# Kernel tuning notes

Hardware: AMD Instinct MI355X
Metric: run time of the kernel (lower is better)

The kernel has to match this reference:

```python
import math
import jax, jax.numpy as jnp
import numpy as np

B, S, E, H = 4, 2048, 1024, 16
HD = E // H  # 64


def setup_inputs() -> dict:
    key = jax.random.key(0)
    ks = jax.random.split(key, 7)
    scale = 1.0 / math.sqrt(E)
    return {
        "x": jax.random.normal(ks[0], (B, S, E), dtype=jnp.float32),
        "Wq": jax.random.normal(ks[1], (H, HD, E), dtype=jnp.float32) * scale,
        "bq": jax.random.normal(ks[2], (H, HD), dtype=jnp.float32) * 0.01,
        "Wk": jax.random.normal(ks[3], (H, HD, E), dtype=jnp.float32) * scale,
        "bk": jax.random.normal(ks[4], (H, HD), dtype=jnp.float32) * 0.01,
        "Wv": jax.random.normal(ks[5], (H, HD, E), dtype=jnp.float32) * scale,
        "bv": jax.random.normal(ks[6], (H, HD), dtype=jnp.float32) * 0.01,
    }


def reference(x, Wq, bq, Wk, bk, Wv, bv):
    b, s, e = x.shape
    h, hd, _ = Wq.shape
    inv_scale = 1.0 / math.sqrt(hd)
    # per-head linear projections (torch Linear: x @ W^T + b), batched over heads
    q = jnp.einsum("bse,hde->bshd", x, Wq) + bq  # [B,S,H,HD]
    k = jnp.einsum("bse,hde->bshd", x, Wk) + bk
    v = jnp.einsum("bse,hde->bshd", x, Wv) + bv
    # causal mask: -inf above diagonal (added before scaling, as in source;
    # -inf * inv_scale is still -inf so math is identical)
    mask = jnp.triu(jnp.full((s, s), -jnp.inf, dtype=x.dtype), k=1)
    scores = (jnp.einsum("bqhd,bkhd->bhqk", q, k) + mask) * inv_scale  # [B,H,S,S]
    attn = jax.nn.softmax(scores, axis=-1)
    out = jnp.einsum("bhqk,bkhd->bqhd", attn, v)  # [B,S,H,HD]
    # concat over heads in head order == reshape with head-major last dims
    return out.reshape(b, s, h * hd)
```

## Files before the change

### kernel.cpp

```cpp
#include <hip/hip_runtime.h>


typedef __bf16 bf16x8 __attribute__((ext_vector_type(8)));
typedef __bf16 bf16x4 __attribute__((ext_vector_type(4)));
typedef float f32x4 __attribute__((ext_vector_type(4)));
typedef unsigned short us8 __attribute__((ext_vector_type(8)));
typedef unsigned short us4 __attribute__((ext_vector_type(4)));

#define Bb 4
#define Ss 2048
#define Ee 1024
#define Hh 16
#define HD 64

#if __has_builtin(__builtin_amdgcn_exp2f)
#define EXP2(x) __builtin_amdgcn_exp2f(x)
#else
#define EXP2(x) exp2f(x)
#endif

__device__ __forceinline__ unsigned short f2bf(float f) {
  union { float f; unsigned u; } v; v.f = f;
  unsigned u = v.u;
  u += 0x7fffu + ((u >> 16) & 1u);
  return (unsigned short)(u >> 16);
}

__device__ __forceinline__ void gl_lds16(const void* g, void* l) {
  __builtin_amdgcn_global_load_lds((const __attribute__((address_space(1))) void*)g,
                                   (__attribute__((address_space(3))) void*)l, 16, 0, 0);
}

#define DSR(d, a, o) asm volatile("ds_read_b128 %0, %1 offset:" #o : "=v"(d) : "v"(a))
#define DSW(a, d, o) asm volatile("ds_write_b64 %0, %1 offset:" #o :: "v"(a), "v"(d) : "memory")
#define LGKM0 asm volatile("s_waitcnt lgkmcnt(0)" ::: "memory"); __builtin_amdgcn_sched_barrier(0)

__global__ __launch_bounds__(256) void cvt_all(const float* __restrict__ x,
                                               const float* __restrict__ wq,
                                               const float* __restrict__ wk,
                                               const float* __restrict__ wv,
                                               unsigned short* __restrict__ xb,
                                               unsigned short* __restrict__ wb) {
  int i = blockIdx.x * 256 + threadIdx.x;
  const float* src; unsigned short* dst; int idx;
  if (i < 2097152)      { src = x;  dst = xb;                idx = i; }
  else if (i < 2359296) { src = wq; dst = wb;                idx = i - 2097152; }
  else if (i < 2621440) { src = wk; dst = wb + 1048576;      idx = i - 2359296; }
  else                  { src = wv; dst = wb + 2 * 1048576;  idx = i - 2621440; }
  float4 f = ((const float4*)src)[idx];
  us4 o = { f2bf(f.x), f2bf(f.y), f2bf(f.z), f2bf(f.w) };
  ((us4*)dst)[idx] = o;
}

__global__ __launch_bounds__(256, 2) void qkv_gemm(const unsigned short* __restrict__ xb,
                                                   const unsigned short* __restrict__ wb_all,
                                                   const float* __restrict__ bq,
                                                   const float* __restrict__ bk,
                                                   const float* __restrict__ bv,
                                                   unsigned short* __restrict__ qkv) {
  const int z = blockIdx.z;
  const unsigned short* wb = wb_all + (size_t)z * (Ee * Ee);
  const float* bias = (z == 0) ? bq : (z == 1) ? bk : bv;
  unsigned short* outb = qkv + (size_t)z * (Bb * Ss * Ee);
  const float osc = (z == 0) ? 0.180336880f : 1.0f;

  __shared__ unsigned short SMEM[32768];

  const int t = threadIdx.x;
  const int wave = t >> 6, lane = t & 63, quad = lane >> 4, ln = lane & 15;
  const int wr = wave >> 1, wc = wave & 1;
  const int m0 = blockIdx.x * 128, n0 = blockIdx.y * 128;

  const int r32 = t >> 3;
  const int cs = ((t & 7) ^ (r32 & 7)) * 8;
  const int t8 = t * 8;
  const unsigned short* gA0 = xb + (size_t)(m0 + r32) * Ee + cs;
  const unsigned short* gA1 = gA0 + 64 * Ee;
  const unsigned short* gB0 = wb + (size_t)(n0 + r32) * Ee + cs;
  const unsigned short* gB1 = gB0 + 64 * Ee;

  const int swz0 = ((0 * 4 + quad) ^ (ln & 7)) * 16;
  const int swz1 = ((1 * 4 + quad) ^ (ln & 7)) * 16;
  int aA0 = (wr * 32 + ln) * 128 + swz0;
  int aA1 = (wr * 32 + ln) * 128 + swz1;
  int bA0 = 16384 + (wc * 32 + ln) * 128 + swz0;
  int bA1 = 16384 + (wc * 32 + ln) * 128 + swz1;

  f32x4 acc[2][2][2][2] = {};
  bf16x8 af[2][2], bf0[2][2], bf1[2][2];

  gl_lds16(gA0,           &SMEM[t8]);
  gl_lds16(gA0 + 32 * Ee, &SMEM[t8 + 2048]);
  gl_lds16(gB0,           &SMEM[8192 + t8]);
  gl_lds16(gB0 + 32 * Ee, &SMEM[8192 + t8 + 2048]);
  gl_lds16(gB1,           &SMEM[12288 + t8]);
  gl_lds16(gB1 + 32 * Ee, &SMEM[12288 + t8 + 2048]);
  gl_lds16(gA1,           &SMEM[4096 + t8]);
  gl_lds16(gA1 + 32 * Ee, &SMEM[4096 + t8 + 2048]);

#pragma unroll 1
  for (int kt = 0; kt < 15; ++kt) {
    const int sbuf = ((kt & 1) << 14) ^ 16384;
    const int co = (kt + 1) * 64;

    asm volatile("s_waitcnt vmcnt(4)" ::: "memory");
    asm volatile("s_barrier" ::: "memory");
    DSR(af[0][0], aA0, 0);    DSR(af[1][0], aA0, 2048);
    DSR(af[0][1], aA1, 0);    DSR(af[1][1], aA1, 2048);
    DSR(bf0[0][0], bA0, 0);   DSR(bf0[1][0], bA0, 2048);
    DSR(bf0[0][1], bA1, 0);   DSR(bf0[1][1], bA1, 2048);
    gl_lds16(gA0 + co,           &SMEM[sbuf + t8]);
    gl_lds16(gA0 + co + 32 * Ee, &SMEM[sbuf + t8 + 2048]);
    asm volatile("s_barrier" ::: "memory");
    asm volatile("s_waitcnt lgkmcnt(0)" ::: "memory");
    __builtin_amdgcn_sched_barrier(0);
    __builtin_amdgcn_s_setprio(1);
#pragma unroll
    for (int kk = 0; kk < 2; ++kk)
#pragma unroll
      for (int i = 0; i < 2; ++i)
#pragma unroll
        for (int j = 0; j < 2; ++j)
          acc[0][0][i][j] = __builtin_amdgcn_mfma_f32_16x16x32_bf16(af[i][kk], bf0[j][kk], acc[0][0][i][j], 0, 0, 0);
    __builtin_amdgcn_s_setprio(0);
    __builtin_amdgcn_sched_barrier(0);

    asm volatile("s_waitcnt vmcnt(4)" ::: "memory");
    asm volatile("s_barrier" ::: "memory");
    DSR(bf1[0][0], bA0, 8192); DSR(bf1[1][0], bA0, 10240);
    DSR(bf1[0][1], bA1, 8192); DSR(bf1[1][1], bA1, 10240);
    gl_lds16(gB0 + co,           &SMEM[sbuf + 8192 + t8]);
    gl_lds16(gB0 + co + 32 * Ee, &SMEM[sbuf + 8192 + t8 + 2048]);
    asm volatile("s_barrier" ::: "memory");
    asm volatile("s_waitcnt lgkmcnt(0)" ::: "memory");
    __builtin_amdgcn_sched_barrier(0);
    __builtin_amdgcn_s_setprio(1);
#pragma unroll
    for (int kk = 0; kk < 2; ++kk)
#pragma unroll
      for (int i = 0; i < 2; ++i)
#pragma unroll
        for (int j = 0; j < 2; ++j)
          acc[0][1][i][j] = __builtin_amdgcn_mfma_f32_16x16x32_bf16(af[i][kk], bf1[j][kk], acc[0][1][i][j], 0, 0, 0);
    __builtin_amdgcn_s_setprio(0);
    __builtin_amdgcn_sched_barrier(0);

    asm volatile("s_waitcnt vmcnt(4)" ::: "memory");
    asm volatile("s_barrier" ::: "memory");
    DSR(af[0][0], aA0, 8192); DSR(af[1][0], aA0, 10240);
    DSR(af[0][1], aA1, 8192); DSR(af[1][1], aA1, 10240);
    gl_lds16(gB1 + co,           &SMEM[sbuf + 12288 + t8]);
    gl_lds16(gB1 + co + 32 * Ee, &SMEM[sbuf + 12288 + t8 + 2048]);
    asm volatile("s_barrier" ::: "memory");
    asm volatile("s_waitcnt lgkmcnt(0)" ::: "memory");
    __builtin_amdgcn_sched_barrier(0);
    __builtin_amdgcn_s_setprio(1);
#pragma unroll
    for (int kk = 0; kk < 2; ++kk)
#pragma unroll
      for (int i = 0; i < 2; ++i)
#pragma unroll
        for (int j = 0; j < 2; ++j)
          acc[1][0][i][j] = __builtin_amdgcn_mfma_f32_16x16x32_bf16(af[i][kk], bf0[j][kk], acc[1][0][i][j], 0, 0, 0);
    __builtin_amdgcn_s_setprio(0);
    __builtin_amdgcn_sched_barrier(0);

    asm volatile("s_barrier" ::: "memory");
    gl_lds16(gA1 + co,           &SMEM[sbuf + 4096 + t8]);
    gl_lds16(gA1 + co + 32 * Ee, &SMEM[sbuf + 4096 + t8 + 2048]);
    asm volatile("s_barrier" ::: "memory");
    __builtin_amdgcn_sched_barrier(0);
    __builtin_amdgcn_s_setprio(1);
#pragma unroll
    for (int kk = 0; kk < 2; ++kk)
#pragma unroll
      for (int i = 0; i < 2; ++i)
#pragma unroll
        for (int j = 0; j < 2; ++j)
          acc[1][1][i][j] = __builtin_amdgcn_mfma_f32_16x16x32_bf16(af[i][kk], bf1[j][kk], acc[1][1][i][j], 0, 0, 0);
    __builtin_amdgcn_s_setprio(0);
    __builtin_amdgcn_sched_barrier(0);

    aA0 ^= 32768; aA1 ^= 32768; bA0 ^= 32768; bA1 ^= 32768;
  }

  {
    asm volatile("s_waitcnt vmcnt(0)" ::: "memory");
    asm volatile("s_barrier" ::: "memory");
    DSR(af[0][0], aA0, 0);    DSR(af[1][0], aA0, 2048);
    DSR(af[0][1], aA1, 0);    DSR(af[1][1], aA1, 2048);
    DSR(bf0[0][0], bA0, 0);   DSR(bf0[1][0], bA0, 2048);
    DSR(bf0[0][1], bA1, 0);   DSR(bf0[1][1], bA1, 2048);
    DSR(bf1[0][0], bA0, 8192); DSR(bf1[1][0], bA0, 10240);
    DSR(bf1[0][1], bA1, 8192); DSR(bf1[1][1], bA1, 10240);
    asm volatile("s_waitcnt lgkmcnt(0)" ::: "memory");
    __builtin_amdgcn_sched_barrier(0);
#pragma unroll
    for (int kk = 0; kk < 2; ++kk)
#pragma unroll
      for (int i = 0; i < 2; ++i)
#pragma unroll
        for (int j = 0; j < 2; ++j) {
          acc[0][0][i][j] = __builtin_amdgcn_mfma_f32_16x16x32_bf16(af[i][kk], bf0[j][kk], acc[0][0][i][j], 0, 0, 0);
          acc[0][1][i][j] = __builtin_amdgcn_mfma_f32_16x16x32_bf16(af[i][kk], bf1[j][kk], acc[0][1][i][j], 0, 0, 0);
        }
    __builtin_amdgcn_sched_barrier(0);
    DSR(af[0][0], aA0, 8192); DSR(af[1][0], aA0, 10240);
    DSR(af[0][1], aA1, 8192); DSR(af[1][1], aA1, 10240);
    asm volatile("s_waitcnt lgkmcnt(0)" ::: "memory");
    __builtin_amdgcn_sched_barrier(0);
#pragma unroll
    for (int kk = 0; kk < 2; ++kk)
#pragma unroll
      for (int i = 0; i < 2; ++i)
#pragma unroll
        for (int j = 0; j < 2; ++j) {
          acc[1][0][i][j] = __builtin_amdgcn_mfma_f32_16x16x32_bf16(af[i][kk], bf0[j][kk], acc[1][0][i][j], 0, 0, 0);
          acc[1][1][i][j] = __builtin_amdgcn_mfma_f32_16x16x32_bf16(af[i][kk], bf1[j][kk], acc[1][1][i][j], 0, 0, 0);
        }
    __builtin_amdgcn_sched_barrier(0);
  }

  float biasj[2][2];
#pragma unroll
  for (int qb = 0; qb < 2; ++qb)
#pragma unroll
    for (int j = 0; j < 2; ++j)
      biasj[qb][j] = bias[n0 + qb * 64 + wc * 32 + j * 16 + ln];

  if (z != 2) {
#pragma unroll
    for (int qa = 0; qa < 2; ++qa)
#pragma unroll
      for (int qb = 0; qb < 2; ++qb)
#pragma unroll
        for (int i = 0; i < 2; ++i)
#pragma unroll
          for (int j = 0; j < 2; ++j)
#pragma unroll
            for (int r = 0; r < 4; ++r) {
              int m = m0 + qa * 64 + wr * 32 + i * 16 + quad * 4 + r;
              int n = n0 + qb * 64 + wc * 32 + j * 16 + ln;
              int b_ = m >> 11, s = m & 2047;
              int h = n >> 6, d = n & 63;
              outb[(((size_t)b_ * Hh + h) * Ss + s) * HD + d] =
                  f2bf((acc[qa][qb][i][j][r] + biasj[qb][j]) * osc);
            }
  } else {
    __syncthreads();
#pragma unroll
    for (int qa = 0; qa < 2; ++qa)
#pragma unroll
      for (int qb = 0; qb < 2; ++qb)
#pragma unroll
        for (int i = 0; i < 2; ++i)
#pragma unroll
          for (int j = 0; j < 2; ++j)
#pragma unroll
            for (int r = 0; r < 4; ++r) {
              int nc = qb * 64 + wc * 32 + j * 16 + ln;
              int mr = qa * 64 + wr * 32 + i * 16 + quad * 4 + r;
              SMEM[nc * 136 + mr] = f2bf(acc[qa][qb][i][j][r] + biasj[qb][j]);
            }
    __syncthreads();
    int nr = t >> 1, mh = t & 1;
    int n = n0 + nr, h = n >> 6, d = n & 63;
    int b_ = m0 >> 11;
    int s0 = (m0 & 2047) + mh * 64;
#pragma unroll
    for (int q = 0; q < 8; ++q) {
      us8 vdat = *(const us8*)&SMEM[nr * 136 + mh * 64 + q * 8];
      *(us8*)&outb[(((size_t)b_ * Hh + h) * HD + d) * Ss + s0 + q * 8] = vdat;
    }
  }
}

__global__ __launch_bounds__(512, 2) void flash_attn(const unsigned short* __restrict__ qkv,
                                                     float* __restrict__ out) {
  const int id = blockIdx.x;
  const int bh = id & 63;
  const int p = id >> 6;
  const int b_ = bh >> 4, h = bh & 15;

  const unsigned short* qb  = qkv + (size_t)bh * (Ss * HD);
  const unsigned short* kb  = qkv + (size_t)(64 + bh) * (Ss * HD);
  const unsigned short* vtb = qkv + (size_t)(128 + bh) * (Ss * HD);

  __shared__ __bf16 LDS[25600];

  const int t = threadIdx.x;
  const int wave = t >> 6, lane = t & 63, quad = lane >> 4, ln = lane & 15;
  const int uw = wave >> 2;

  const int r6 = t >> 3;
  const int cstage = ((t & 7) ^ (r6 & 7)) * 8;
  const int t8 = t * 8;

  const int qts[2] = { 15 - p, p };
  const int KTB = 2 * qts[0] + 2;
  const int su0 = 2 * qts[0] + uw;
  const int su1 = 2 * qts[1] + uw;
  const int qrow0 = qts[0] * 128 + wave * 16 + ln;
  const int qrow1 = qts[1] * 128 + wave * 16 + ln;

  int ka0 = ln * 128 + ((quad ^ (ln & 7)) * 16);
  int ka1 = ln * 128 + (((4 + quad) ^ (ln & 7)) * 16);
  const int pw = (16384 + (wave * 16 + ln) * 72 + quad * 4) * 2;
  const int pr = (16384 + (wave * 16 + ln) * 72 + quad * 8) * 2;

  bf16x8 qf[2][2];
#pragma unroll
  for (int qt = 0; qt < 2; ++qt)
#pragma unroll
    for (int ks = 0; ks < 2; ++ks)
      qf[qt][ks] = *(const bf16x8*)(qb + (size_t)(qts[qt] * 128 + wave * 16 + ln) * HD +
                                    ks * 32 + quad * 8);

  bf16x8 onef;
#pragma unroll
  for (int j = 0; j < 8; ++j) onef[j] = (__bf16)1.0f;

  f32x4 o[2][4] = {};
  f32x4 l4[2] = {};

  auto body = [&](int kt) {
    if (kt > su0) return;
    const bool a1 = (kt <= su1);
    const int k0 = kt * 64;
    f32x4 s0[4] = {}, s1[4] = {};
    bf16x8 kf[2][2];

    DSR(kf[0][0], ka0, 0);    DSR(kf[1][0], ka0, 2048);
    DSR(kf[0][1], ka1, 0);    DSR(kf[1][1], ka1, 2048);
    LGKM0;
#pragma unroll
    for (int ks = 0; ks < 2; ++ks) {
      s0[0] = __builtin_amdgcn_mfma_f32_16x16x32_bf16(kf[0][ks], qf[0][ks], s0[0], 0, 0, 0);
      s0[1] = __builtin_amdgcn_mfma_f32_16x16x32_bf16(kf[1][ks], qf[0][ks], s0[1], 0, 0, 0);
    }
    if (a1)
#pragma unroll
      for (int ks = 0; ks < 2; ++ks) {
        s1[0] = __builtin_amdgcn_mfma_f32_16x16x32_bf16(kf[0][ks], qf[1][ks], s1[0], 0, 0, 0);
        s1[1] = __builtin_amdgcn_mfma_f32_16x16x32_bf16(kf[1][ks], qf[1][ks], s1[1], 0, 0, 0);
      }
    DSR(kf[0][0], ka0, 4096); DSR(kf[1][0], ka0, 6144);
    DSR(kf[0][1], ka1, 4096); DSR(kf[1][1], ka1, 6144);
    LGKM0;
#pragma unroll
    for (int ks = 0; ks < 2; ++ks) {
      s0[2] = __builtin_amdgcn_mfma_f32_16x16x32_bf16(kf[0][ks], qf[0][ks], s0[2], 0, 0, 0);
      s0[3] = __builtin_amdgcn_mfma_f32_16x16x32_bf16(kf[1][ks], qf[0][ks], s0[3], 0, 0, 0);
    }
    if (a1)
#pragma unroll
      for (int ks = 0; ks < 2; ++ks) {
        s1[2] = __builtin_amdgcn_mfma_f32_16x16x32_bf16(kf[0][ks], qf[1][ks], s1[2], 0, 0, 0);
        s1[3] = __builtin_amdgcn_mfma_f32_16x16x32_bf16(kf[1][ks], qf[1][ks], s1[3], 0, 0, 0);
      }

    if (kt == su0) {
#pragma unroll
      for (int g = 0; g < 4; ++g)
#pragma unroll
        for (int r = 0; r < 4; ++r) {
          int kcol = k0 + g * 16 + quad * 4 + r;
          if (kcol > qrow0) s0[g][r] = -__builtin_inff();
        }
    }
    {
      bf16x4 pk;
      pk = bf16x4{ (__bf16)EXP2(s0[0][0]), (__bf16)EXP2(s0[0][1]), (__bf16)EXP2(s0[0][2]), (__bf16)EXP2(s0[0][3]) };
      DSW(pw, pk, 0);
      pk = bf16x4{ (__bf16)EXP2(s0[1][0]), (__bf16)EXP2(s0[1][1]), (__bf16)EXP2(s0[1][2]), (__bf16)EXP2(s0[1][3]) };
      DSW(pw, pk, 32);
      pk = bf16x4{ (__bf16)EXP2(s0[2][0]), (__bf16)EXP2(s0[2][1]), (__bf16)EXP2(s0[2][2]), (__bf16)EXP2(s0[2][3]) };
      DSW(pw, pk, 64);
      pk = bf16x4{ (__bf16)EXP2(s0[3][0]), (__bf16)EXP2(s0[3][1]), (__bf16)EXP2(s0[3][2]), (__bf16)EXP2(s0[3][3]) };
      DSW(pw, pk, 96);
    }
    bf16x8 pf0[2], pf1[2];
    DSR(pf0[0], pr, 0); DSR(pf0[1], pr, 64);
    LGKM0;

    if (a1) {
      if (kt == su1) {
#pragma unroll
        for (int g = 0; g < 4; ++g)
#pragma unroll
          for (int r = 0; r < 4; ++r) {
            int kcol = k0 + g * 16 + quad * 4 + r;
            if (kcol > qrow1) s1[g][r] = -__builtin_inff();
          }
      }
      bf16x4 pk;
      pk = bf16x4{ (__bf16)EXP2(s1[0][0]), (__bf16)EXP2(s1[0][1]), (__bf16)EXP2(s1[0][2]), (__bf16)EXP2(s1[0][3]) };
      DSW(pw, pk, 0);
      pk = bf16x4{ (__bf16)EXP2(s1[1][0]), (__bf16)EXP2(s1[1][1]), (__bf16)EXP2(s1[1][2]), (__bf16)EXP2(s1[1][3]) };
      DSW(pw, pk, 32);
      pk = bf16x4{ (__bf16)EXP2(s1[2][0]), (__bf16)EXP2(s1[2][1]), (__bf16)EXP2(s1[2][2]), (__bf16)EXP2(s1[2][3]) };
      DSW(pw, pk, 64);
      pk = bf16x4{ (__bf16)EXP2(s1[3][0]), (__bf16)EXP2(s1[3][1]), (__bf16)EXP2(s1[3][2]), (__bf16)EXP2(s1[3][3]) };
      DSW(pw, pk, 96);
      DSR(pf1[0], pr, 0); DSR(pf1[1], pr, 64);
      LGKM0;
    }

    l4[0] = __builtin_amdgcn_mfma_f32_16x16x32_bf16(pf0[0], onef, l4[0], 0, 0, 0);
    l4[0] = __builtin_amdgcn_mfma_f32_16x16x32_bf16(pf0[1], onef, l4[0], 0, 0, 0);
    if (a1) {
      l4[1] = __builtin_amdgcn_mfma_f32_16x16x32_bf16(pf1[0], onef, l4[1], 0, 0, 0);
      l4[1] = __builtin_amdgcn_mfma_f32_16x16x32_bf16(pf1[1], onef, l4[1], 0, 0, 0);
    }

    DSR(kf[0][0], ka0, 16384); DSR(kf[1][0], ka0, 18432);
    DSR(kf[0][1], ka1, 16384); DSR(kf[1][1], ka1, 18432);
    LGKM0;
#pragma unroll
    for (int ks = 0; ks < 2; ++ks) {
      o[0][0] = __builtin_amdgcn_mfma_f32_16x16x32_bf16(pf0[ks], kf[0][ks], o[0][0], 0, 0, 0);
      o[0][1] = __builtin_amdgcn_mfma_f32_16x16x32_bf16(pf0[ks], kf[1][ks], o[0][1], 0, 0, 0);
    }
    if (a1)
#pragma unroll
      for (int ks = 0; ks < 2; ++ks) {
        o[1][0] = __builtin_amdgcn_mfma_f32_16x16x32_bf16(pf1[ks], kf[0][ks], o[1][0], 0, 0, 0);
        o[1][1] = __builtin_amdgcn_mfma_f32_16x16x32_bf16(pf1[ks], kf[1][ks], o[1][1], 0, 0, 0);
      }
    DSR(kf[0][0], ka0, 20480); DSR(kf[1][0], ka0, 22528);
    DSR(kf[0][1], ka1, 20480); DSR(kf[1][1], ka1, 22528);
    LGKM0;
#pragma unroll
    for (int ks = 0; ks < 2; ++ks) {
      o[0][2] = __builtin_amdgcn_mfma_f32_16x16x32_bf16(pf0[ks], kf[0][ks], o[0][2], 0, 0, 0);
      o[0][3] = __builtin_amdgcn_mfma_f32_16x16x32_bf16(pf0[ks], kf[1][ks], o[0][3], 0, 0, 0);
    }
    if (a1)
#pragma unroll
      for (int ks = 0; ks < 2; ++ks) {
        o[1][2] = __builtin_amdgcn_mfma_f32_16x16x32_bf16(pf1[ks], kf[0][ks], o[1][2], 0, 0, 0);
        o[1][3] = __builtin_amdgcn_mfma_f32_16x16x32_bf16(pf1[ks], kf[1][ks], o[1][3], 0, 0, 0);
      }
  };

  gl_lds16(kb + r6 * HD + cstage,  &LDS[t8]);
  gl_lds16(vtb + r6 * Ss + cstage, &LDS[8192 + t8]);

#pragma unroll 1
  for (int kt = 0; kt < KTB - 1; ++kt) {
    const int sb = (kt & 1) ^ 1;
    gl_lds16(kb + (size_t)(kt + 1) * (64 * HD) + r6 * HD + cstage, &LDS[sb * 4096 + t8]);
    gl_lds16(vtb + (kt + 1) * 64 + r6 * Ss + cstage,               &LDS[8192 + sb * 4096 + t8]);
    asm volatile("s_waitcnt vmcnt(2)" ::: "memory");
    asm volatile("s_barrier" ::: "memory");
    body(kt);
    asm volatile("s_barrier" ::: "memory");
    ka0 ^= 8192; ka1 ^= 8192;
  }
  asm volatile("s_waitcnt vmcnt(0)" ::: "memory");
  asm volatile("s_barrier" ::: "memory");
  body(KTB - 1);

#pragma unroll
  for (int qt = 0; qt < 2; ++qt) {
    float linv[4];
#pragma unroll
    for (int r = 0; r < 4; ++r) linv[r] = 1.0f / l4[qt][r];
#pragma unroll
    for (int g = 0; g < 4; ++g)
#pragma unroll
      for (int r = 0; r < 4; ++r) {
        int orow = qts[qt] * 128 + wave * 16 + quad * 4 + r;
        out[((size_t)b_ * Ss + orow) * Ee + h * HD + g * 16 + ln] = o[qt][g][r] * linv[r];
      }
  }
}

extern "C" void kernel_launch(void* const* d_in, const int* in_sizes, int n_in,
                              void* d_out, int out_size, void* d_ws, size_t ws_size,
                              hipStream_t stream) {
  const float* x  = (const float*)d_in[0];
  const float* Wq = (const float*)d_in[1];
  const float* bq = (const float*)d_in[2];
  const float* Wk = (const float*)d_in[3];
  const float* bk = (const float*)d_in[4];
  const float* Wv = (const float*)d_in[5];
  const float* bv = (const float*)d_in[6];
  float* out = (float*)d_out;

  unsigned short* ws  = (unsigned short*)d_ws;
  unsigned short* xb  = ws;
  unsigned short* wb  = ws + 8388608;
  unsigned short* qkv = ws + 8388608 + 3 * 1048576;

  cvt_all<<<11264, 256, 0, stream>>>(x, Wq, Wk, Wv, xb, wb);
  qkv_gemm<<<dim3(64, 8, 3), 256, 0, stream>>>(xb, wb, bq, bk, bv, qkv);
  flash_attn<<<512, 512, 0, stream>>>(qkv, out);
}
```

Before: 199.9 us.

## Collapse four-phase GEMM mainloop into single-phase prefetch-all then compute

Reworks the projection GEMM main loop from a four-phase interleaved schedule into one phase per k-tile. Each iteration first issues all eight global-to-LDS prefetches for the next tile, waits for the current tile, loads all A and B fragments from LDS at once, then runs all 32 MFMAs back to back. This cuts the number of barriers and waits per iteration. In exchange it holds more fragment registers live (separate af0/af1) and loses the finer-grained overlap between LDS reads and MFMAs.

```diff
diff --git a/kernel.cpp b/kernel.cpp
--- a/kernel.cpp
+++ b/kernel.cpp
@@ -87,7 +87,7 @@
   int bA1 = 16384 + (wc * 32 + ln) * 128 + swz1;
 
   f32x4 acc[2][2][2][2] = {};
-  bf16x8 af[2][2], bf0[2][2], bf1[2][2];
+  bf16x8 af0[2][2], af1[2][2], bf0[2][2], bf1[2][2];
 
   gl_lds16(gA0,           &SMEM[t8]);
   gl_lds16(gA0 + 32 * Ee, &SMEM[t8 + 2048]);
@@ -103,17 +103,27 @@
     const int sbuf = ((kt & 1) << 14) ^ 16384;
     const int co = (kt + 1) * 64;
 
-    asm volatile("s_waitcnt vmcnt(4)" ::: "memory");
-    asm volatile("s_barrier" ::: "memory");
-    DSR(af[0][0], aA0, 0);    DSR(af[1][0], aA0, 2048);
-    DSR(af[0][1], aA1, 0);    DSR(af[1][1], aA1, 2048);
-    DSR(bf0[0][0], bA0, 0);   DSR(bf0[1][0], bA0, 2048);
-    DSR(bf0[0][1], bA1, 0);   DSR(bf0[1][1], bA1, 2048);
     gl_lds16(gA0 + co,           &SMEM[sbuf + t8]);
     gl_lds16(gA0 + co + 32 * Ee, &SMEM[sbuf + t8 + 2048]);
+    gl_lds16(gB0 + co,           &SMEM[sbuf + 8192 + t8]);
+    gl_lds16(gB0 + co + 32 * Ee, &SMEM[sbuf + 8192 + t8 + 2048]);
+    gl_lds16(gB1 + co,           &SMEM[sbuf + 12288 + t8]);
+    gl_lds16(gB1 + co + 32 * Ee, &SMEM[sbuf + 12288 + t8 + 2048]);
+    gl_lds16(gA1 + co,           &SMEM[sbuf + 4096 + t8]);
+    gl_lds16(gA1 + co + 32 * Ee, &SMEM[sbuf + 4096 + t8 + 2048]);
+
+    asm volatile("s_waitcnt vmcnt(8)" ::: "memory");
     asm volatile("s_barrier" ::: "memory");
-    asm volatile("s_waitcnt lgkmcnt(0)" ::: "memory");
-    __builtin_amdgcn_sched_barrier(0);
+
+    DSR(af0[0][0], aA0, 0);    DSR(af0[1][0], aA0, 2048);
+    DSR(af0[0][1], aA1, 0);    DSR(af0[1][1], aA1, 2048);
+    DSR(af1[0][0], aA0, 8192); DSR(af1[1][0], aA0, 10240);
+    DSR(af1[0][1], aA1, 8192); DSR(af1[1][1], aA1, 10240);
+    DSR(bf0[0][0], bA0, 0);    DSR(bf0[1][0], bA0, 2048);
+    DSR(bf0[0][1], bA1, 0);    DSR(bf0[1][1], bA1, 2048);
+    DSR(bf1[0][0], bA0, 8192); DSR(bf1[1][0], bA0, 10240);
+    DSR(bf1[0][1], bA1, 8192); DSR(bf1[1][1], bA1, 10240);
+    LGKM0;
     __builtin_amdgcn_s_setprio(1);
 #pragma unroll
     for (int kk = 0; kk < 2; ++kk)
@@ -121,65 +131,31 @@
       for (int i = 0; i < 2; ++i)
 #pragma unroll
         for (int j = 0; j < 2; ++j)
-          acc[0][0][i][j] = __builtin_amdgcn_mfma_f32_16x16x32_bf16(af[i][kk], bf0[j][kk], acc[0][0][i][j], 0, 0, 0);
+          acc[0][0][i][j] = __builtin_amdgcn_mfma_f32_16x16x32_bf16(af0[i][kk], bf0[j][kk], acc[0][0][i][j], 0, 0, 0);
+#pragma unroll
+    for (int kk = 0; kk < 2; ++kk)
+#pragma unroll
+      for (int i = 0; i < 2; ++i)
+#pragma unroll
+        for (int j = 0; j < 2; ++j)
+          acc[0][1][i][j] = __builtin_amdgcn_mfma_f32_16x16x32_bf16(af0[i][kk], bf1[j][kk], acc[0][1][i][j], 0, 0, 0);
+#pragma unroll
+    for (int kk = 0; kk < 2; ++kk)
+#pragma unroll
+      for (int i = 0; i < 2; ++i)
+#pragma unroll
+        for (int j = 0; j < 2; ++j)
+          acc[1][0][i][j] = __builtin_amdgcn_mfma_f32_16x16x32_bf16(af1[i][kk], bf0[j][kk], acc[1][0][i][j], 0, 0, 0);
+#pragma unroll
+    for (int kk = 0; kk < 2; ++kk)
+#pragma unroll
+      for (int i = 0; i < 2; ++i)
+#pragma unroll
+        for (int j = 0; j < 2; ++j)
+          acc[1][1][i][j] = __builtin_amdgcn_mfma_f32_16x16x32_bf16(af1[i][kk], bf1[j][kk], acc[1][1][i][j], 0, 0, 0);
     __builtin_amdgcn_s_setprio(0);
     __builtin_amdgcn_sched_barrier(0);
-
-    asm volatile("s_waitcnt vmcnt(4)" ::: "memory");
     asm volatile("s_barrier" ::: "memory");
-    DSR(bf1[0][0], bA0, 8192); DSR(bf1[1][0], bA0, 10240);
-    DSR(bf1[0][1], bA1, 8192); DSR(bf1[1][1], bA1, 10240);
-    gl_lds16(gB0 + co,           &SMEM[sbuf + 8192 + t8]);
-    gl_lds16(gB0 + co + 32 * Ee, &SMEM[sbuf + 8192 + t8 + 2048]);
-    asm volatile("s_barrier" ::: "memory");
-    asm volatile("s_waitcnt lgkmcnt(0)" ::: "memory");
-    __builtin_amdgcn_sched_barrier(0);
-    __builtin_amdgcn_s_setprio(1);
-#pragma unroll
-    for (int kk = 0; kk < 2; ++kk)
-#pragma unroll
-      for (int i = 0; i < 2; ++i)
-#pragma unroll
-        for (int j = 0; j < 2; ++j)
-          acc[0][1][i][j] = __builtin_amdgcn_mfma_f32_16x16x32_bf16(af[i][kk], bf1[j][kk], acc[0][1][i][j], 0, 0, 0);
-    __builtin_amdgcn_s_setprio(0);
-    __builtin_amdgcn_sched_barrier(0);
-
-    asm volatile("s_waitcnt vmcnt(4)" ::: "memory");
-    asm volatile("s_barrier" ::: "memory");
-    DSR(af[0][0], aA0, 8192); DSR(af[1][0], aA0, 10240);
-    DSR(af[0][1], aA1, 8192); DSR(af[1][1], aA1, 10240);
-    gl_lds16(gB1 + co,           &SMEM[sbuf + 12288 + t8]);
-    gl_lds16(gB1 + co + 32 * Ee, &SMEM[sbuf + 12288 + t8 + 2048]);
-    asm volatile("s_barrier" ::: "memory");
-    asm volatile("s_waitcnt lgkmcnt(0)" ::: "memory");
-    __builtin_amdgcn_sched_barrier(0);
-    __builtin_amdgcn_s_setprio(1);
-#pragma unroll
-    for (int kk = 0; kk < 2; ++kk)
-#pragma unroll
-      for (int i = 0; i < 2; ++i)
-#pragma unroll
-        for (int j = 0; j < 2; ++j)
-          acc[1][0][i][j] = __builtin_amdgcn_mfma_f32_16x16x32_bf16(af[i][kk], bf0[j][kk], acc[1][0][i][j], 0, 0, 0);
-    __builtin_amdgcn_s_setprio(0);
-    __builtin_amdgcn_sched_barrier(0);
-
-    asm volatile("s_barrier" ::: "memory");
-    gl_lds16(gA1 + co,           &SMEM[sbuf + 4096 + t8]);
-    gl_lds16(gA1 + co + 32 * Ee, &SMEM[sbuf + 4096 + t8 + 2048]);
-    asm volatile("s_barrier" ::: "memory");
-    __builtin_amdgcn_sched_barrier(0);
-    __builtin_amdgcn_s_setprio(1);
-#pragma unroll
-    for (int kk = 0; kk < 2; ++kk)
-#pragma unroll
-      for (int i = 0; i < 2; ++i)
-#pragma unroll
-        for (int j = 0; j < 2; ++j)
-          acc[1][1][i][j] = __builtin_amdgcn_mfma_f32_16x16x32_bf16(af[i][kk], bf1[j][kk], acc[1][1][i][j], 0, 0, 0);
-    __builtin_amdgcn_s_setprio(0);
-    __builtin_amdgcn_sched_barrier(0);
 
     aA0 ^= 32768; aA1 ^= 32768; bA0 ^= 32768; bA1 ^= 32768;
   }
@@ -187,37 +163,43 @@
   {
     asm volatile("s_waitcnt vmcnt(0)" ::: "memory");
     asm volatile("s_barrier" ::: "memory");
-    DSR(af[0][0], aA0, 0);    DSR(af[1][0], aA0, 2048);
-    DSR(af[0][1], aA1, 0);    DSR(af[1][1], aA1, 2048);
-    DSR(bf0[0][0], bA0, 0);   DSR(bf0[1][0], bA0, 2048);
-    DSR(bf0[0][1], bA1, 0);   DSR(bf0[1][1], bA1, 2048);
+    DSR(af0[0][0], aA0, 0);    DSR(af0[1][0], aA0, 2048);
+    DSR(af0[0][1], aA1, 0);    DSR(af0[1][1], aA1, 2048);
+    DSR(af1[0][0], aA0, 8192); DSR(af1[1][0], aA0, 10240);
+    DSR(af1[0][1], aA1, 8192); DSR(af1[1][1], aA1, 10240);
+    DSR(bf0[0][0], bA0, 0);    DSR(bf0[1][0], bA0, 2048);
+    DSR(bf0[0][1], bA1, 0);    DSR(bf0[1][1], bA1, 2048);
     DSR(bf1[0][0], bA0, 8192); DSR(bf1[1][0], bA0, 10240);
     DSR(bf1[0][1], bA1, 8192); DSR(bf1[1][1], bA1, 10240);
-    asm volatile("s_waitcnt lgkmcnt(0)" ::: "memory");
-    __builtin_amdgcn_sched_barrier(0);
-#pragma unroll
-    for (int kk = 0; kk < 2; ++kk)
-#pragma unroll
-      for (int i = 0; i < 2; ++i)
-#pragma unroll
-        for (int j = 0; j < 2; ++j) {
-          acc[0][0][i][j] = __builtin_amdgcn_mfma_f32_16x16x32_bf16(af[i][kk], bf0[j][kk], acc[0][0][i][j], 0, 0, 0);
-          acc[0][1][i][j] = __builtin_amdgcn_mfma_f32_16x16x32_bf16(af[i][kk], bf1[j][kk], acc[0][1][i][j], 0, 0, 0);
-        }
-    __builtin_amdgcn_sched_barrier(0);
-    DSR(af[0][0], aA0, 8192); DSR(af[1][0], aA0, 10240);
-    DSR(af[0][1], aA1, 8192); DSR(af[1][1], aA1, 10240);
-    asm volatile("s_waitcnt lgkmcnt(0)" ::: "memory");
-    __builtin_amdgcn_sched_barrier(0);
-#pragma unroll
-    for (int kk = 0; kk < 2; ++kk)
-#pragma unroll
-      for (int i = 0; i < 2; ++i)
-#pragma unroll
-        for (int j = 0; j < 2; ++j) {
-          acc[1][0][i][j] = __builtin_amdgcn_mfma_f32_16x16x32_bf16(af[i][kk], bf0[j][kk], acc[1][0][i][j], 0, 0, 0);
-          acc[1][1][i][j] = __builtin_amdgcn_mfma_f32_16x16x32_bf16(af[i][kk], bf1[j][kk], acc[1][1][i][j], 0, 0, 0);
-        }
+    LGKM0;
+#pragma unroll
+    for (int kk = 0; kk < 2; ++kk)
+#pragma unroll
+      for (int i = 0; i < 2; ++i)
+#pragma unroll
+        for (int j = 0; j < 2; ++j)
+          acc[0][0][i][j] = __builtin_amdgcn_mfma_f32_16x16x32_bf16(af0[i][kk], bf0[j][kk], acc[0][0][i][j], 0, 0, 0);
+#pragma unroll
+    for (int kk = 0; kk < 2; ++kk)
+#pragma unroll
+      for (int i = 0; i < 2; ++i)
+#pragma unroll
+        for (int j = 0; j < 2; ++j)
+          acc[0][1][i][j] = __builtin_amdgcn_mfma_f32_16x16x32_bf16(af0[i][kk], bf1[j][kk], acc[0][1][i][j], 0, 0, 0);
+#pragma unroll
+    for (int kk = 0; kk < 2; ++kk)
+#pragma unroll
+      for (int i = 0; i < 2; ++i)
+#pragma unroll
+        for (int j = 0; j < 2; ++j)
+          acc[1][0][i][j] = __builtin_amdgcn_mfma_f32_16x16x32_bf16(af1[i][kk], bf0[j][kk], acc[1][0][i][j], 0, 0, 0);
+#pragma unroll
+    for (int kk = 0; kk < 2; ++kk)
+#pragma unroll
+      for (int i = 0; i < 2; ++i)
+#pragma unroll
+        for (int j = 0; j < 2; ++j)
+          acc[1][1][i][j] = __builtin_amdgcn_mfma_f32_16x16x32_bf16(af1[i][kk], bf1[j][kk], acc[1][1][i][j], 0, 0, 0);
     __builtin_amdgcn_sched_barrier(0);
   }
 
```

New measurement: 194.9 us. -2.5%, faster.
